# Kernel tuning notes

Measured on AMD Instinct MI355X. Metric: run time of the kernel, lower is better.

## Reference

```python
import jax, jax.numpy as jnp
import numpy as np

N = 80000          # total nodes
F_IN = 16          # num_features
NUM_GRAPHS = 8
P = N // NUM_GRAPHS
EDGES_PER_GRAPH = 80000   # undirected samples per graph (~avg degree 16 after symmetrize)
OUT_DIM = 20000    # num_nodes (output classes)


def _graclus(src, dst, n, rng):
    """Greedy graclus matching (unweighted): visit nodes in random order, match with
    first unmatched neighbor. Cluster id = min(i, match[i]), relabeled consecutively."""
    perm = np.argsort(src, kind='stable')
    s, d = src[perm], dst[perm]
    starts = np.searchsorted(s, np.arange(n))
    ends = np.searchsorted(s, np.arange(n) + 1)
    match = np.full(n, -1, dtype=np.int64)
    for u in rng.permutation(n):
        if match[u] >= 0:
            continue
        match[u] = u
        for v in d[starts[u]:ends[u]]:
            if v != u and match[v] < 0:
                match[u] = v
                match[v] = u
                break
    rep = np.minimum(np.arange(n), match)
    _, cluster = np.unique(rep, return_inverse=True)
    return cluster.astype(np.int64)


def _pool_edges(src, dst, cluster, n1):
    """max_pool edge pooling: map endpoints to clusters, drop self-loops, coalesce."""
    cs, cd = cluster[src], cluster[dst]
    m = cs != cd
    key = np.unique(cs[m].astype(np.int64) * n1 + cd[m])
    return (key // n1).astype(np.int64), (key % n1).astype(np.int64)


def _glorot(k, shape):
    return jax.random.normal(k, shape, jnp.float32) * (2.0 / (shape[0] + shape[1])) ** 0.5


def setup_inputs() -> dict:
    rng = np.random.default_rng(0)
    srcs, dsts = [], []
    for g in range(NUM_GRAPHS):  # edges only within each graph block
        lo = g * P
        u = rng.integers(0, P, EDGES_PER_GRAPH)
        v = rng.integers(0, P, EDGES_PER_GRAPH)
        m = u != v
        u, v = u[m] + lo, v[m] + lo
        key = np.unique(np.minimum(u, v).astype(np.int64) * N + np.maximum(u, v))
        a, b = key // N, key % N
        srcs += [a, b]
        dsts += [b, a]
    src = np.concatenate(srcs).astype(np.int64)
    dst = np.concatenate(dsts).astype(np.int64)
    batch1 = (np.arange(N) // P).astype(np.int64)

    cluster1 = _graclus(src, dst, N, rng)
    n1 = int(cluster1.max()) + 1
    src2, dst2 = _pool_edges(src, dst, cluster1, n1)
    batch2 = np.zeros(n1, np.int64)
    batch2[cluster1] = batch1
    cluster2 = _graclus(src2, dst2, n1, rng)
    n2 = int(cluster2.max()) + 1
    batch3 = np.zeros(n2, np.int64)
    batch3[cluster2] = batch2

    ks = jax.random.split(jax.random.key(0), 12)
    return dict(
        x=jax.random.normal(ks[0], (N, F_IN), jnp.float32),
        W0a=_glorot(ks[1], (F_IN, 32)), W1a=_glorot(ks[2], (F_IN, 32)),
        b1=jnp.zeros((32,), jnp.float32),
        W0b=_glorot(ks[3], (32, 64)), W1b=_glorot(ks[4], (32, 64)),
        b2=jnp.zeros((64,), jnp.float32),
        fcw1=_glorot(ks[5], (64, 128)), fcb1=jnp.zeros((128,), jnp.float32),
        fcw2=_glorot(ks[6], (128, OUT_DIM)), fcb2=jnp.zeros((OUT_DIM,), jnp.float32),
        edge_index1=jnp.asarray(np.stack([src, dst])),
        cluster1=jnp.asarray(cluster1),
        edge_index2=jnp.asarray(np.stack([src2, dst2])),
        cluster2=jnp.asarray(cluster2),
        batch3=jnp.asarray(batch3),
        n1=n1, n2=n2, n_graphs=NUM_GRAPHS,
    )


def _cheb_relu(x, edge_index, W0, W1, b, n):
    """PyG ChebConv K=2, sym norm, lambda_max=2: out = x@W0 + (L~ x)@W1 + b with
    L~ = L - I = -D^{-1/2} A D^{-1/2}; then ReLU."""
    s, d = edge_index[0], edge_index[1]
    deg = jax.ops.segment_sum(jnp.ones(s.shape[0], x.dtype), d, num_segments=n)
    dinv = jnp.where(deg > 0, deg ** -0.5, 0.0)
    w = -(dinv[s] * dinv[d])                       # [E]
    tx1 = jax.ops.segment_sum(w[:, None] * x[s], d, num_segments=n)  # L~ x
    return jax.nn.relu(x @ W0 + tx1 @ W1 + b)


def reference(x, W0a, W1a, b1, W0b, W1b, b2, fcw1, fcb1, fcw2, fcb2,
              edge_index1, cluster1, edge_index2, cluster2, batch3,
              n1, n2, n_graphs):
    h = _cheb_relu(x, edge_index1, W0a, W1a, b1, x.shape[0])     # [N,32]
    hp = jax.ops.segment_max(h, cluster1, num_segments=n1)        # max_pool -> [n1,32]
    h2 = _cheb_relu(hp, edge_index2, W0b, W1b, b2, n1)            # [n1,64]
    h3 = jax.ops.segment_max(h2, cluster2, num_segments=n2)       # max_pool_x -> [n2,64]
    sums = jax.ops.segment_sum(h3, batch3, num_segments=n_graphs)
    cnt = jax.ops.segment_sum(jnp.ones(h3.shape[0], h3.dtype), batch3, num_segments=n_graphs)
    g = sums / cnt[:, None]                                       # global_mean_pool [G,64]
    g = jax.nn.relu(g @ fcw1 + fcb1)                              # dropout is eval-mode identity
    return g @ fcw2 + fcb2                                        # [G, OUT_DIM]
```

## Files before the change

kernel.cpp:

```cpp
#include <hip/hip_runtime.h>

static inline int idiv(int a, int b) { return (a + b - 1) / b; }

__device__ __forceinline__ int swz8(int bid, int nb) {
    int q = nb >> 3, r = nb & 7;
    int x = bid & 7, c = bid >> 3;
    return (x < r ? x * (q + 1) : r * (q + 1) + (x - r) * q) + c;
}

__global__ void k_zero(float4* __restrict__ p, long n4) {
    long t = (long)blockIdx.x * blockDim.x + threadIdx.x;
    long stride = (long)gridDim.x * blockDim.x;
    for (; t < n4; t += stride) p[t] = make_float4(0.f, 0.f, 0.f, 0.f);
}

__global__ void k_prep1(const int* __restrict__ src, const int* __restrict__ dst,
                        int* __restrict__ ust, int* __restrict__ uen,
                        int* __restrict__ cntS, int E) {
    int e = blockIdx.x * blockDim.x + threadIdx.x;
    if (e >= E) return;
    int s = src[e], d = dst[e];
    if (s >= d) return;
    atomicAdd(&cntS[d], 1);
    bool prevup = false; int ps = -1;
    if (e > 0) { ps = src[e - 1]; prevup = (ps < dst[e - 1]); }
    if (e == 0 || !prevup || ps != s) ust[s] = e;
    bool nextup = false; int ns = -1;
    if (e + 1 < E) { ns = src[e + 1]; nextup = (ns < dst[e + 1]); }
    if (e + 1 == E || !nextup || ns != s) uen[s] = e + 1;
}

__global__ void k_bounds2(const int* __restrict__ src, int* __restrict__ rs,
                          int* __restrict__ re, int E) {
    int e = blockIdx.x * blockDim.x + threadIdx.x;
    if (e >= E) return;
    int s = src[e];
    if (e == 0 || src[e - 1] != s) rs[s] = e;
    if (e + 1 == E || src[e + 1] != s) re[s] = e + 1;
}

__global__ void k_dinv1(const int* __restrict__ cntS, const int* __restrict__ ust,
                        const int* __restrict__ uen, float* __restrict__ dinv, int n) {
    int t = blockIdx.x * blockDim.x + threadIdx.x;
    if (t < n) {
        int deg = cntS[t] + uen[t] - ust[t];
        dinv[t] = (deg > 0) ? rsqrtf((float)deg) : 0.0f;
    }
}

__global__ void k_dinv2(const int* __restrict__ rs, const int* __restrict__ re,
                        float* __restrict__ dinv, int n) {
    int t = blockIdx.x * blockDim.x + threadIdx.x;
    if (t < n) {
        int deg = re[t] - rs[t];
        dinv[t] = (deg > 0) ? rsqrtf((float)deg) : 0.0f;
    }
}

__global__ void k_scan_blk(const int* __restrict__ cnt, int* __restrict__ offs,
                           int* __restrict__ blksum, int n) {
    __shared__ int ts[256];
    int blk = blockIdx.x;
    int tid = threadIdx.x;
    int i0 = blk * 1024 + tid * 4;
    int a0 = 0, a1 = 0, a2 = 0, a3 = 0;
    if (i0 + 3 < n) {
        int4 v = *(const int4*)&cnt[i0];
        a0 = v.x; a1 = v.y; a2 = v.z; a3 = v.w;
    } else {
        if (i0 + 0 < n) a0 = cnt[i0 + 0];
        if (i0 + 1 < n) a1 = cnt[i0 + 1];
        if (i0 + 2 < n) a2 = cnt[i0 + 2];
    }
    int tsum = a0 + a1 + a2 + a3;
    ts[tid] = tsum;
    __syncthreads();
    for (int off = 1; off < 256; off <<= 1) {
        int v = (tid >= off) ? ts[tid - off] : 0;
        __syncthreads();
        ts[tid] += v;
        __syncthreads();
    }
    int ex = ts[tid] - tsum;
    if (tid == 255) blksum[blk] = ts[255];
    int p0 = ex, p1 = ex + a0, p2 = p1 + a1, p3 = p2 + a2;
    if (i0 + 3 < n) {
        *(int4*)&offs[i0] = make_int4(p0, p1, p2, p3);
    } else {
        if (i0 + 0 < n) offs[i0 + 0] = p0;
        if (i0 + 1 < n) offs[i0 + 1] = p1;
        if (i0 + 2 < n) offs[i0 + 2] = p2;
    }
}

__global__ void k_scan_tot(int* __restrict__ blksum, int nblk) {
    __shared__ int s[1024];
    int tid = threadIdx.x;
    int v = (tid < nblk) ? blksum[tid] : 0;
    s[tid] = v;
    __syncthreads();
    for (int off = 1; off < 1024; off <<= 1) {
        int t = (tid >= off) ? s[tid - off] : 0;
        __syncthreads();
        s[tid] += t;
        __syncthreads();
    }
    if (tid < nblk) blksum[tid] = s[tid] - v;
}

__global__ void k_scan_add(int* __restrict__ offs, int* __restrict__ cursor,
                           const int* __restrict__ blksum, int n) {
    int t = blockIdx.x * blockDim.x + threadIdx.x;
    if (t < n) {
        int v = offs[t] + blksum[t >> 10];
        offs[t] = v;
        cursor[t] = v;
    }
}

__global__ void k_fillS(const int* __restrict__ src, const int* __restrict__ dst,
                        int* __restrict__ cursor, int* __restrict__ csr, int E) {
    int e = blockIdx.x * blockDim.x + threadIdx.x;
    if (e >= E) return;
    int s = src[e], d = dst[e];
    if (s < d) {
        int pos = atomicAdd(&cursor[d], 1);
        csr[pos] = s;
    }
}

template <int LOGF>
__global__ void k_gather1(const int* __restrict__ ust, const int* __restrict__ uen,
                          const int* __restrict__ dst1, const int* __restrict__ offsS,
                          const int* __restrict__ cntS, const int* __restrict__ csrS,
                          const float* __restrict__ dinv, const float* __restrict__ xin,
                          float* __restrict__ tx, int n) {
    int vb = swz8(blockIdx.x, gridDim.x);
    int t = vb * blockDim.x + threadIdx.x;
    int d = t >> LOGF, f = t & ((1 << LOGF) - 1);
    if (d >= n) return;
    float acc = 0.0f;
    int e = ust[d], e1 = uen[d];
    for (; e + 3 < e1; e += 4) {
        int s0 = dst1[e], s1 = dst1[e + 1], s2 = dst1[e + 2], s3 = dst1[e + 3];
        float v0 = dinv[s0] * xin[((long)s0 << LOGF) + f];
        float v1 = dinv[s1] * xin[((long)s1 << LOGF) + f];
        float v2 = dinv[s2] * xin[((long)s2 << LOGF) + f];
        float v3 = dinv[s3] * xin[((long)s3 << LOGF) + f];
        acc += (v0 + v1) + (v2 + v3);
    }
    for (; e < e1; e++) {
        int s = dst1[e];
        acc += dinv[s] * xin[((long)s << LOGF) + f];
    }
    int i = offsS[d], i1 = i + cntS[d];
    for (; i + 3 < i1; i += 4) {
        int s0 = csrS[i], s1 = csrS[i + 1], s2 = csrS[i + 2], s3 = csrS[i + 3];
        float v0 = dinv[s0] * xin[((long)s0 << LOGF) + f];
        float v1 = dinv[s1] * xin[((long)s1 << LOGF) + f];
        float v2 = dinv[s2] * xin[((long)s2 << LOGF) + f];
        float v3 = dinv[s3] * xin[((long)s3 << LOGF) + f];
        acc += (v0 + v1) + (v2 + v3);
    }
    for (; i < i1; i++) {
        int s = csrS[i];
        acc += dinv[s] * xin[((long)s << LOGF) + f];
    }
    tx[((long)d << LOGF) + f] = -dinv[d] * acc;
}

template <int LOGF>
__global__ void k_gather2(const int* __restrict__ rs, const int* __restrict__ re,
                          const int* __restrict__ dst2, const float* __restrict__ dinv,
                          const float* __restrict__ xin, float* __restrict__ tx, int n) {
    int vb = swz8(blockIdx.x, gridDim.x);
    int t = vb * blockDim.x + threadIdx.x;
    int d = t >> LOGF, f = t & ((1 << LOGF) - 1);
    if (d >= n) return;
    float acc = 0.0f;
    int j = rs[d], j1 = re[d];
    for (; j + 3 < j1; j += 4) {
        int s0 = dst2[j], s1 = dst2[j + 1], s2 = dst2[j + 2], s3 = dst2[j + 3];
        float v0 = dinv[s0] * xin[((long)s0 << LOGF) + f];
        float v1 = dinv[s1] * xin[((long)s1 << LOGF) + f];
        float v2 = dinv[s2] * xin[((long)s2 << LOGF) + f];
        float v3 = dinv[s3] * xin[((long)s3 << LOGF) + f];
        acc += (v0 + v1) + (v2 + v3);
    }
    for (; j < j1; j++) {
        int s = dst2[j];
        acc += dinv[s] * xin[((long)s << LOGF) + f];
    }
    tx[((long)d << LOGF) + f] = -dinv[d] * acc;
}

__global__ void k_cheb1_max(const float* __restrict__ x, const float* __restrict__ tx,
                            const float* __restrict__ W0, const float* __restrict__ W1,
                            const float* __restrict__ b, const int* __restrict__ cl,
                            float* __restrict__ hp, int N) {
    __shared__ float sW0[16 * 32], sW1[16 * 32], sb[32];
    for (int i = threadIdx.x; i < 16 * 32; i += blockDim.x) {
        sW0[i] = W0[i];
        sW1[i] = W1[i];
    }
    if (threadIdx.x < 32) sb[threadIdx.x] = b[threadIdx.x];
    __syncthreads();
    int t = blockIdx.x * blockDim.x + threadIdx.x;
    int n = t >> 5, j = t & 31;
    if (n >= N) return;
    const float* xr = x + (long)n * 16;
    const float* tr = tx + (long)n * 16;
    float acc = sb[j];
#pragma unroll
    for (int k = 0; k < 16; k++) acc += xr[k] * sW0[k * 32 + j] + tr[k] * sW1[k * 32 + j];
    float v = fmaxf(acc, 0.0f);
    atomicMax((int*)&hp[((long)cl[n] << 5) + j], __float_as_int(v));
}

__global__ void k_cheb2_max(const float* __restrict__ xp, const float* __restrict__ tx,
                            const float* __restrict__ W0, const float* __restrict__ W1,
                            const float* __restrict__ b, const int* __restrict__ cl,
                            float* __restrict__ h3, int n1) {
    __shared__ float sW0[32 * 64], sW1[32 * 64], sb[64];
    for (int i = threadIdx.x; i < 32 * 64; i += blockDim.x) {
        sW0[i] = W0[i];
        sW1[i] = W1[i];
    }
    if (threadIdx.x < 64) sb[threadIdx.x] = b[threadIdx.x];
    __syncthreads();
    int t = blockIdx.x * blockDim.x + threadIdx.x;
    int n = t >> 6, j = t & 63;
    if (n >= n1) return;
    const float* xr = xp + (long)n * 32;
    const float* tr = tx + (long)n * 32;
    float acc = sb[j];
#pragma unroll
    for (int k = 0; k < 32; k++) acc += xr[k] * sW0[k * 64 + j] + tr[k] * sW1[k * 64 + j];
    float v = fmaxf(acc, 0.0f);
    atomicMax((int*)&h3[((long)cl[n] << 6) + j], __float_as_int(v));
}

__global__ void k_gsum(const float* __restrict__ h3, const int* __restrict__ batch,
                       float* __restrict__ gsum, float* __restrict__ gcnt, int n2) {
    __shared__ float s[8 * 64];
    __shared__ float sc[8];
    for (int i = threadIdx.x; i < 512; i += blockDim.x) s[i] = 0.0f;
    if (threadIdx.x < 8) sc[threadIdx.x] = 0.0f;
    __syncthreads();
    long total = (long)n2 * 64;
    long stride = (long)gridDim.x * blockDim.x;
    for (long t = (long)blockIdx.x * blockDim.x + threadIdx.x; t < total; t += stride) {
        int n = (int)(t >> 6), f = (int)(t & 63);
        int g = batch[n];
        atomicAdd(&s[g * 64 + f], h3[t]);
        if (f == 0) atomicAdd(&sc[g], 1.0f);
    }
    __syncthreads();
    for (int i = threadIdx.x; i < 512; i += blockDim.x) atomicAdd(&gsum[i], s[i]);
    if (threadIdx.x < 8) atomicAdd(&gcnt[threadIdx.x], sc[threadIdx.x]);
}

__global__ void k_fc1(const float* __restrict__ gsum, const float* __restrict__ gcnt,
                      const float* __restrict__ fcw1, const float* __restrict__ fcb1,
                      float* __restrict__ g1) {
    __shared__ float sg[8 * 64];
    int tid = threadIdx.x;
    if (tid < 512) {
        float c = gcnt[tid >> 6];
        sg[tid] = (c > 0.0f) ? gsum[tid] / c : 0.0f;
    }
    __syncthreads();
    int gi = tid >> 7, j = tid & 127;
    float acc = fcb1[j];
#pragma unroll 8
    for (int k = 0; k < 64; k++) acc += sg[gi * 64 + k] * fcw1[k * 128 + j];
    g1[tid] = fmaxf(acc, 0.0f);
}

__global__ void k_fc2(const float* __restrict__ g1, const float* __restrict__ fcw2,
                      const float* __restrict__ fcb2, float* __restrict__ out, int OUT) {
    __shared__ float sg[8 * 128];
    for (int i = threadIdx.x; i < 1024; i += blockDim.x) sg[i] = g1[i];
    __syncthreads();
    int o = blockIdx.x * blockDim.x + threadIdx.x;
    if (o >= OUT) return;
    float bias = fcb2[o];
    float acc[8];
#pragma unroll
    for (int gi = 0; gi < 8; gi++) acc[gi] = bias;
    for (int k = 0; k < 128; k++) {
        float w = fcw2[(long)k * OUT + o];
#pragma unroll
        for (int gi = 0; gi < 8; gi++) acc[gi] += sg[gi * 128 + k] * w;
    }
#pragma unroll
    for (int gi = 0; gi < 8; gi++) out[(long)gi * OUT + o] = acc[gi];
}

extern "C" void kernel_launch(void* const* d_in, const int* in_sizes, int n_in,
                              void* d_out, int out_size, void* d_ws, size_t ws_size,
                              hipStream_t stream) {
    const float* x    = (const float*)d_in[0];
    const float* W0a  = (const float*)d_in[1];
    const float* W1a  = (const float*)d_in[2];
    const float* b1   = (const float*)d_in[3];
    const float* W0b  = (const float*)d_in[4];
    const float* W1b  = (const float*)d_in[5];
    const float* b2   = (const float*)d_in[6];
    const float* fcw1 = (const float*)d_in[7];
    const float* fcb1 = (const float*)d_in[8];
    const float* fcw2 = (const float*)d_in[9];
    const float* fcb2 = (const float*)d_in[10];
    const int* ei1    = (const int*)d_in[11];
    const int* cl1    = (const int*)d_in[12];
    const int* ei2    = (const int*)d_in[13];
    const int* cl2    = (const int*)d_in[14];
    const int* b3     = (const int*)d_in[15];

    const int N  = in_sizes[12];
    const int E1 = in_sizes[11] / 2;
    const int E2 = in_sizes[13] / 2;
    const int n1 = in_sizes[14];
    const int n2 = in_sizes[15];
    const int G  = 8;
    const int OUT = out_size / G;

    const int nmax = (N > n1) ? N : n1;

    auto rnd = [](size_t b) { return (b + 255) & ~(size_t)255; };
    size_t cntB  = rnd((size_t)N * 4);
    size_t ustB  = rnd((size_t)N * 4);
    size_t uenB  = rnd((size_t)N * 4);
    size_t rs2B  = rnd((size_t)n1 * 4);
    size_t re2B  = rnd((size_t)n1 * 4);
    size_t hpB   = rnd((size_t)n1 * 32 * 4);
    size_t h3B   = rnd((size_t)n2 * 64 * 4);
    size_t smlB  = rnd((512 + 8 + 1024) * 4);
    size_t offB  = rnd((size_t)N * 4);
    size_t curB  = rnd((size_t)N * 4);
    size_t csrB  = rnd((size_t)(E1 / 2 + 64) * 4);
    size_t dinvB = rnd((size_t)nmax * 4);
    size_t blkB  = rnd((size_t)1024 * 4);

    char* base = (char*)d_ws;
    char* p = base;
    int*   cntS   = (int*)p;           p += cntB;
    int*   ust    = (int*)p;           p += ustB;
    int*   uen    = (int*)p;           p += uenB;
    int*   rs2    = (int*)p;           p += rs2B;
    int*   re2    = (int*)p;           p += re2B;
    float* hp     = (float*)p;         p += hpB;
    float* h3     = (float*)p;         p += h3B;
    float* gsum   = (float*)p;         p += smlB;
    float* gcnt   = gsum + 512;
    float* g1     = gcnt + 8;
    size_t zeroB  = (size_t)(p - base);
    int*   offsS  = (int*)p;           p += offB;
    int*   cursorS= (int*)p;           p += curB;
    int*   csrS   = (int*)p;           p += csrB;
    float* dinv   = (float*)p;         p += dinvB;
    int*   blksum = (int*)p;           p += blkB;
    float* txA    = (float*)p;
    (void)ws_size;

    dim3 B(256);
    {
        long n4 = (long)(zeroB / 16);
        int g = idiv((int)((n4 < 1048576) ? n4 : 1048576), 256);
        if (g < 1) g = 1;
        if (g > 4096) g = 4096;
        k_zero<<<g, B, 0, stream>>>((float4*)base, n4);
    }

    {
        int nblk = idiv(N, 1024);
        k_prep1<<<idiv(E1, 256), B, 0, stream>>>(ei1, ei1 + E1, ust, uen, cntS, E1);
        k_dinv1<<<idiv(N, 256), B, 0, stream>>>(cntS, ust, uen, dinv, N);
        k_scan_blk<<<nblk, B, 0, stream>>>(cntS, offsS, blksum, N);
        k_scan_tot<<<1, 1024, 0, stream>>>(blksum, nblk);
        k_scan_add<<<idiv(N, 256), B, 0, stream>>>(offsS, cursorS, blksum, N);
        k_fillS<<<idiv(E1, 256), B, 0, stream>>>(ei1, ei1 + E1, cursorS, csrS, E1);
        k_gather1<4><<<idiv(N * 16, 256), B, 0, stream>>>(ust, uen, ei1 + E1, offsS, cntS, csrS,
                                                          dinv, x, txA, N);
        k_cheb1_max<<<idiv(N * 32, 256), B, 0, stream>>>(x, txA, W0a, W1a, b1, cl1, hp, N);
    }

    {
        k_bounds2<<<idiv(E2, 256), B, 0, stream>>>(ei2, rs2, re2, E2);
        k_dinv2<<<idiv(n1, 256), B, 0, stream>>>(rs2, re2, dinv, n1);
        k_gather2<5><<<idiv(n1 * 32, 256), B, 0, stream>>>(rs2, re2, ei2 + E2, dinv, hp, txA, n1);
        k_cheb2_max<<<idiv(n1 * 64, 256), B, 0, stream>>>(hp, txA, W0b, W1b, b2, cl2, h3, n1);
    }

    int gb = idiv(n2 * 64, 256);
    if (gb > 256) gb = 256;
    k_gsum<<<gb, B, 0, stream>>>(h3, b3, gsum, gcnt, n2);
    k_fc1<<<1, 1024, 0, stream>>>(gsum, gcnt, fcw1, fcb1, g1);
    k_fc2<<<idiv(OUT, 256), B, 0, stream>>>(g1, fcw2, fcb2, (float*)d_out, OUT);
}
```

Baseline: 222.0 us.

## Replace atomicMax pooling with per-cluster member lists and direct writes

Adds a pass that records up to two member nodes per cluster. The Chebyshev layers then run one thread group per cluster, take the max over those members and write the pooled row directly. This removes the float-as-int atomicMax scatter and the need to zero the hp/h3 buffers, and it also swizzles block order. It relies on graclus clusters holding at most two nodes, and the extra member-count kernels add launches.

```diff
diff --git a/kernel.cpp b/kernel.cpp
--- a/kernel.cpp
+++ b/kernel.cpp
@@ -55,6 +55,15 @@
         int deg = re[t] - rs[t];
         dinv[t] = (deg > 0) ? rsqrtf((float)deg) : 0.0f;
     }
+}
+
+__global__ void k_members(const int* __restrict__ cl, int* __restrict__ mcnt,
+                          int* __restrict__ mem, int n) {
+    int t = blockIdx.x * blockDim.x + threadIdx.x;
+    if (t >= n) return;
+    int c = cl[t];
+    int slot = atomicAdd(&mcnt[c], 1);
+    if (slot < 2) mem[2 * c + slot] = t;
 }
 
 __global__ void k_scan_blk(const int* __restrict__ cnt, int* __restrict__ offs,
@@ -194,10 +203,10 @@
     tx[((long)d << LOGF) + f] = -dinv[d] * acc;
 }
 
-__global__ void k_cheb1_max(const float* __restrict__ x, const float* __restrict__ tx,
-                            const float* __restrict__ W0, const float* __restrict__ W1,
-                            const float* __restrict__ b, const int* __restrict__ cl,
-                            float* __restrict__ hp, int N) {
+__global__ void k_cheb1_pool(const float* __restrict__ x, const float* __restrict__ tx,
+                             const float* __restrict__ W0, const float* __restrict__ W1,
+                             const float* __restrict__ b, const int* __restrict__ mcnt,
+                             const int* __restrict__ mem, float* __restrict__ hp, int n1) {
     __shared__ float sW0[16 * 32], sW1[16 * 32], sb[32];
     for (int i = threadIdx.x; i < 16 * 32; i += blockDim.x) {
         sW0[i] = W0[i];
@@ -205,22 +214,33 @@
     }
     if (threadIdx.x < 32) sb[threadIdx.x] = b[threadIdx.x];
     __syncthreads();
-    int t = blockIdx.x * blockDim.x + threadIdx.x;
-    int n = t >> 5, j = t & 31;
-    if (n >= N) return;
-    const float* xr = x + (long)n * 16;
-    const float* tr = tx + (long)n * 16;
+    int vb = swz8(blockIdx.x, gridDim.x);
+    int t = vb * blockDim.x + threadIdx.x;
+    int c = t >> 5, j = t & 31;
+    if (c >= n1) return;
+    int m0 = mem[2 * c];
+    const float* xr = x + (long)m0 * 16;
+    const float* tr = tx + (long)m0 * 16;
     float acc = sb[j];
 #pragma unroll
     for (int k = 0; k < 16; k++) acc += xr[k] * sW0[k * 32 + j] + tr[k] * sW1[k * 32 + j];
-    float v = fmaxf(acc, 0.0f);
-    atomicMax((int*)&hp[((long)cl[n] << 5) + j], __float_as_int(v));
-}
-
-__global__ void k_cheb2_max(const float* __restrict__ xp, const float* __restrict__ tx,
-                            const float* __restrict__ W0, const float* __restrict__ W1,
-                            const float* __restrict__ b, const int* __restrict__ cl,
-                            float* __restrict__ h3, int n1) {
+    float best = fmaxf(acc, 0.0f);
+    if (mcnt[c] > 1) {
+        int m1 = mem[2 * c + 1];
+        const float* xr1 = x + (long)m1 * 16;
+        const float* tr1 = tx + (long)m1 * 16;
+        float a1 = sb[j];
+#pragma unroll
+        for (int k = 0; k < 16; k++) a1 += xr1[k] * sW0[k * 32 + j] + tr1[k] * sW1[k * 32 + j];
+        best = fmaxf(best, fmaxf(a1, 0.0f));
+    }
+    hp[((long)c << 5) + j] = best;
+}
+
+__global__ void k_cheb2_pool(const float* __restrict__ xp, const float* __restrict__ tx,
+                             const float* __restrict__ W0, const float* __restrict__ W1,
+                             const float* __restrict__ b, const int* __restrict__ mcnt,
+                             const int* __restrict__ mem, float* __restrict__ h3, int n2) {
     __shared__ float sW0[32 * 64], sW1[32 * 64], sb[64];
     for (int i = threadIdx.x; i < 32 * 64; i += blockDim.x) {
         sW0[i] = W0[i];
@@ -228,16 +248,27 @@
     }
     if (threadIdx.x < 64) sb[threadIdx.x] = b[threadIdx.x];
     __syncthreads();
-    int t = blockIdx.x * blockDim.x + threadIdx.x;
-    int n = t >> 6, j = t & 63;
-    if (n >= n1) return;
-    const float* xr = xp + (long)n * 32;
-    const float* tr = tx + (long)n * 32;
+    int vb = swz8(blockIdx.x, gridDim.x);
+    int t = vb * blockDim.x + threadIdx.x;
+    int c = t >> 6, j = t & 63;
+    if (c >= n2) return;
+    int m0 = mem[2 * c];
+    const float* xr = xp + (long)m0 * 32;
+    const float* tr = tx + (long)m0 * 32;
     float acc = sb[j];
 #pragma unroll
     for (int k = 0; k < 32; k++) acc += xr[k] * sW0[k * 64 + j] + tr[k] * sW1[k * 64 + j];
-    float v = fmaxf(acc, 0.0f);
-    atomicMax((int*)&h3[((long)cl[n] << 6) + j], __float_as_int(v));
+    float best = fmaxf(acc, 0.0f);
+    if (mcnt[c] > 1) {
+        int m1 = mem[2 * c + 1];
+        const float* xr1 = xp + (long)m1 * 32;
+        const float* tr1 = tx + (long)m1 * 32;
+        float a1 = sb[j];
+#pragma unroll
+        for (int k = 0; k < 32; k++) a1 += xr1[k] * sW0[k * 64 + j] + tr1[k] * sW1[k * 64 + j];
+        best = fmaxf(best, fmaxf(a1, 0.0f));
+    }
+    h3[((long)c << 6) + j] = best;
 }
 
 __global__ void k_gsum(const float* __restrict__ h3, const int* __restrict__ batch,
@@ -333,14 +364,18 @@
     size_t uenB  = rnd((size_t)N * 4);
     size_t rs2B  = rnd((size_t)n1 * 4);
     size_t re2B  = rnd((size_t)n1 * 4);
-    size_t hpB   = rnd((size_t)n1 * 32 * 4);
-    size_t h3B   = rnd((size_t)n2 * 64 * 4);
+    size_t mc1B  = rnd((size_t)n1 * 4);
+    size_t mc2B  = rnd((size_t)n2 * 4);
     size_t smlB  = rnd((512 + 8 + 1024) * 4);
     size_t offB  = rnd((size_t)N * 4);
     size_t curB  = rnd((size_t)N * 4);
     size_t csrB  = rnd((size_t)(E1 / 2 + 64) * 4);
     size_t dinvB = rnd((size_t)nmax * 4);
     size_t blkB  = rnd((size_t)1024 * 4);
+    size_t mem1B = rnd((size_t)n1 * 2 * 4);
+    size_t mem2B = rnd((size_t)n2 * 2 * 4);
+    size_t hpB   = rnd((size_t)n1 * 32 * 4);
+    size_t h3B   = rnd((size_t)n2 * 64 * 4);
 
     char* base = (char*)d_ws;
     char* p = base;
@@ -349,8 +384,8 @@
     int*   uen    = (int*)p;           p += uenB;
     int*   rs2    = (int*)p;           p += rs2B;
     int*   re2    = (int*)p;           p += re2B;
-    float* hp     = (float*)p;         p += hpB;
-    float* h3     = (float*)p;         p += h3B;
+    int*   mcnt1  = (int*)p;           p += mc1B;
+    int*   mcnt2  = (int*)p;           p += mc2B;
     float* gsum   = (float*)p;         p += smlB;
     float* gcnt   = gsum + 512;
     float* g1     = gcnt + 8;
@@ -360,6 +395,10 @@
     int*   csrS   = (int*)p;           p += csrB;
     float* dinv   = (float*)p;         p += dinvB;
     int*   blksum = (int*)p;           p += blkB;
+    int*   mem1   = (int*)p;           p += mem1B;
+    int*   mem2   = (int*)p;           p += mem2B;
+    float* hp     = (float*)p;         p += hpB;
+    float* h3     = (float*)p;         p += h3B;
     float* txA    = (float*)p;
     (void)ws_size;
 
@@ -375,6 +414,7 @@
     {
         int nblk = idiv(N, 1024);
         k_prep1<<<idiv(E1, 256), B, 0, stream>>>(ei1, ei1 + E1, ust, uen, cntS, E1);
+        k_members<<<idiv(N, 256), B, 0, stream>>>(cl1, mcnt1, mem1, N);
         k_dinv1<<<idiv(N, 256), B, 0, stream>>>(cntS, ust, uen, dinv, N);
         k_scan_blk<<<nblk, B, 0, stream>>>(cntS, offsS, blksum, N);
         k_scan_tot<<<1, 1024, 0, stream>>>(blksum, nblk);
@@ -382,14 +422,15 @@
         k_fillS<<<idiv(E1, 256), B, 0, stream>>>(ei1, ei1 + E1, cursorS, csrS, E1);
         k_gather1<4><<<idiv(N * 16, 256), B, 0, stream>>>(ust, uen, ei1 + E1, offsS, cntS, csrS,
                                                           dinv, x, txA, N);
-        k_cheb1_max<<<idiv(N * 32, 256), B, 0, stream>>>(x, txA, W0a, W1a, b1, cl1, hp, N);
+        k_cheb1_pool<<<idiv(n1 * 32, 256), B, 0, stream>>>(x, txA, W0a, W1a, b1, mcnt1, mem1, hp, n1);
     }
 
     {
         k_bounds2<<<idiv(E2, 256), B, 0, stream>>>(ei2, rs2, re2, E2);
+        k_members<<<idiv(n1, 256), B, 0, stream>>>(cl2, mcnt2, mem2, n1);
         k_dinv2<<<idiv(n1, 256), B, 0, stream>>>(rs2, re2, dinv, n1);
         k_gather2<5><<<idiv(n1 * 32, 256), B, 0, stream>>>(rs2, re2, ei2 + E2, dinv, hp, txA, n1);
-        k_cheb2_max<<<idiv(n1 * 64, 256), B, 0, stream>>>(hp, txA, W0b, W1b, b2, cl2, h3, n1);
+        k_cheb2_pool<<<idiv(n2 * 64, 256), B, 0, stream>>>(hp, txA, W0b, W1b, b2, mcnt2, mem2, h3, n2);
     }
 
     int gb = idiv(n2 * 64, 256);
```

After: 240.2 us. 1.08x slower.
